# Kernel tuning notes

Hardware: AMD Instinct MI355X
Metric: run time of the kernel (lower is better)

## Reference

```python
import jax, jax.numpy as jnp
import numpy as np

B, T, K, D, H, HL, S, KN = 4096, 50, 32, 64, 256, 128, 100000, 1000


def setup_inputs() -> dict:
    key = jax.random.key(0)
    ks = jax.random.split(key, 24)
    inp = {
        "uididx": jax.random.randint(ks[0], (B,), 0, S, dtype=jnp.int32),
        "kcodeidx": jax.random.randint(ks[1], (B, K), 0, KN, dtype=jnp.int32),
        "kcode_len": jax.random.randint(ks[2], (B,), 1, K + 1, dtype=jnp.int32),
        "qidemb": jax.random.normal(ks[3], (B, T, D), dtype=jnp.float32),
        "qid_len": jax.random.randint(ks[4], (B,), 1, T + 1, dtype=jnp.int32),
        # embedding tables
        "stuE": jax.random.normal(ks[5], (S, D), dtype=jnp.float32) * 0.1,
        "knE": jax.random.normal(ks[6], (KN, D), dtype=jnp.float32) * 0.1,
        # Theta DNN params
        "T_W1": jax.random.normal(ks[7], (D, H), dtype=jnp.float32) * (1.0 / np.sqrt(D)),
        "T_b1": jnp.zeros((H,), jnp.float32),
        "T_W2": jax.random.normal(ks[8], (H, 1), dtype=jnp.float32) * (1.0 / np.sqrt(H)),
        "T_b2": jnp.zeros((1,), jnp.float32),
        # A DNN params
        "A_W1": jax.random.normal(ks[9], (D, H), dtype=jnp.float32) * (1.0 / np.sqrt(D)),
        "A_b1": jnp.zeros((H,), jnp.float32),
        "A_W2": jax.random.normal(ks[10], (H, 1), dtype=jnp.float32) * (1.0 / np.sqrt(H)),
        "A_b2": jnp.zeros((1,), jnp.float32),
        # LSTM params (gate order i,f,g,o) + output head
        "L_Wi": jax.random.normal(ks[11], (D, 4 * HL), dtype=jnp.float32) * (1.0 / np.sqrt(D)),
        "L_Wh": jax.random.normal(ks[12], (HL, 4 * HL), dtype=jnp.float32) * (1.0 / np.sqrt(HL)),
        "L_b": jnp.zeros((4 * HL,), jnp.float32),
        "L_Wo": jax.random.normal(ks[13], (HL, 1), dtype=jnp.float32) * (1.0 / np.sqrt(HL)),
        "L_bo": jnp.zeros((1,), jnp.float32),
    }
    return inp


def _dnn(x, W1, b1, W2, b2):
    return jnp.tanh(x @ W1 + b1) @ W2 + b2


def _lstm_last(x, lengths, Wi, Wh, b):
    # x: [B,T,D]; returns last valid hidden state [B,HL]
    xg = jnp.einsum('btd,dh->bth', x, Wi) + b  # precomputed input projections
    h0 = jnp.zeros((x.shape[0], Wh.shape[0]), x.dtype)

    def step(carry, inp):
        h, c = carry
        g_x, t = inp
        g = g_x + h @ Wh
        i, f, gg, o = jnp.split(g, 4, axis=-1)
        c2 = jax.nn.sigmoid(f) * c + jax.nn.sigmoid(i) * jnp.tanh(gg)
        h2 = jax.nn.sigmoid(o) * jnp.tanh(c2)
        upd = (t < lengths)[:, None]
        return (jnp.where(upd, h2, h), jnp.where(upd, c2, c)), None

    (h, _), _ = jax.lax.scan(step, (h0, h0), (xg.transpose(1, 0, 2), jnp.arange(x.shape[1])))
    return h


def reference(uididx, kcodeidx, kcode_len, qidemb, qid_len, stuE, knE,
              T_W1, T_b1, T_W2, T_b2, A_W1, A_b1, A_W2, A_b2,
              L_Wi, L_Wh, L_b, L_Wo, L_bo):
    stu = stuE[uididx]            # [B,D]
    kemb = knE[kcodeidx]          # [B,K,D]
    kmask = jnp.arange(kcodeidx.shape[1])[None, :] < kcode_len[:, None]  # [B,K]
    kmf = kmask.astype(kemb.dtype)

    # per-student mastery: sigmoid(kemb @ stu / 5), then masked reductions
    mastery = jax.nn.sigmoid(jnp.einsum('bkd,bd->bk', kemb, stu) / 5.0)
    mastvec = jnp.einsum('bk,bkd->bd', mastery * kmf, kemb)  # sum(mastery * kemb)
    avec = jnp.einsum('bk,bkd->bd', kmf, kemb)               # sum(kemb)

    # scaled dot-product attention: q=qidemb, k=v=kemb, scale=0.15
    scores = jnp.einsum('btd,bkd->btk', qidemb, kemb) * 0.15
    scores = jnp.where(kmask[:, None, :], scores, -1e9)
    attw = jax.nn.softmax(scores, axis=-1)
    bvec = jnp.einsum('btk,bkd->btd', attw, kemb)            # [B,T,D]

    t = _dnn(mastvec, T_W1, T_b1, T_W2, T_b2)                             # theta [B,1]
    a = 8.0 * (jax.nn.sigmoid(jnp.abs(_dnn(avec, A_W1, A_b1, A_W2, A_b2))) - 0.5)
    hT = _lstm_last(bvec, qid_len, L_Wi, L_Wh, L_b)
    b = 8.0 * (jax.nn.sigmoid(hT @ L_Wo + L_bo) - 0.5)                    # [B,1]

    return jax.nn.sigmoid(a * (t - b))  # IRT response probability [B,1]
```

## Files before the change

### kernel.cpp

```cpp
#include <hip/hip_runtime.h>
#include <math.h>

#define B_  4096
#define T_  50
#define K_  32
#define D_  64
#define H_  256
#define HL_ 128
#define G4_ 512

typedef __attribute__((ext_vector_type(8))) short bf16x8;
typedef __attribute__((ext_vector_type(4))) float f32x4;

__device__ __forceinline__ float fast_exp(float x){ return __expf(x); }
__device__ __forceinline__ float fast_rcp(float x){ return __builtin_amdgcn_rcpf(x); }
__device__ __forceinline__ float sigmoidf_(float x){ return fast_rcp(1.f + fast_exp(-x)); }
__device__ __forceinline__ float tanhf_(float x){ return 1.f - 2.f*fast_rcp(1.f + fast_exp(2.f*x)); }

__device__ __forceinline__ short f2bf(float f){
  union { float f; unsigned u; } v; v.f = f;
  unsigned r = v.u + 0x7FFFu + ((v.u >> 16) & 1u);
  return (short)(r >> 16);
}
__device__ __forceinline__ float bf2f(short s){
  union { unsigned u; float f; } v; v.u = ((unsigned)(unsigned short)s) << 16;
  return v.f;
}

__device__ __forceinline__ float wave_reduce_sum(float v){
  #pragma unroll
  for (int off = 32; off; off >>= 1) v += __shfl_xor(v, off);
  return v;
}

#define KROW 72
#define PROW 40

__global__ __launch_bounds__(256) void head_kernel(
    const int* __restrict__ uididx, const int* __restrict__ kcodeidx,
    const int* __restrict__ kcode_len, const float* __restrict__ qidemb,
    const int* __restrict__ qid_len, const float* __restrict__ stuE,
    const float* __restrict__ knE,
    const float* __restrict__ T_W1, const float* __restrict__ T_b1,
    const float* __restrict__ T_W2, const float* __restrict__ T_b2,
    const float* __restrict__ A_W1, const float* __restrict__ A_b1,
    const float* __restrict__ A_W2, const float* __restrict__ A_b2,
    short* __restrict__ bvec, float* __restrict__ t_val, float* __restrict__ a_val)
{
  __shared__ __align__(16) short s_kemb[K_*KROW];
  __shared__ __align__(16) short s_kembT[D_*PROW];
  __shared__ __align__(16) short s_p[64*PROW];
  __shared__ float s_stu[D_];
  __shared__ float s_mast[K_];
  __shared__ float s_kmf[K_];
  __shared__ float s_mvec[D_];
  __shared__ float s_avec[D_];
  __shared__ float s_redT[4];
  __shared__ float s_redA[4];

  const int b    = blockIdx.x;
  const int tid  = threadIdx.x;
  const int lane = tid & 63;
  const int w    = tid >> 6;
  const int l15  = lane & 15;
  const int quad = lane >> 4;
  const int klen = kcode_len[b];
  const int qlen = qid_len[b];

  if (tid < D_) s_stu[tid] = stuE[uididx[b]*D_ + tid];
  #pragma unroll
  for (int i = tid; i < 512; i += 256){
    int k = i >> 4, f4 = i & 15;
    const float4 v = *(const float4*)&knE[(size_t)kcodeidx[b*K_ + k]*D_ + f4*4];
    short4 b4; b4.x = f2bf(v.x); b4.y = f2bf(v.y); b4.z = f2bf(v.z); b4.w = f2bf(v.w);
    *(short4*)&s_kemb[k*KROW + f4*4] = b4;
    int d = f4*4;
    s_kembT[(d+0)*PROW + k] = b4.x;
    s_kembT[(d+1)*PROW + k] = b4.y;
    s_kembT[(d+2)*PROW + k] = b4.z;
    s_kembT[(d+3)*PROW + k] = b4.w;
  }
  __syncthreads();

  {
    int k = tid >> 3, l8 = tid & 7;
    float s = 0.f;
    #pragma unroll
    for (int j = 0; j < 8; ++j){
      int d = l8 + 8*((j + k) & 7);
      s += s_stu[d] * bf2f(s_kemb[k*KROW + d]);
    }
    s += __shfl_xor(s, 1); s += __shfl_xor(s, 2); s += __shfl_xor(s, 4);
    if (l8 == 0){
      float valid = (k < klen) ? 1.f : 0.f;
      s_mast[k] = valid * sigmoidf_(s * 0.2f);
      s_kmf[k]  = valid;
    }
  }
  __syncthreads();

  if (tid < D_){
    float mv = 0.f, av = 0.f;
    #pragma unroll 4
    for (int k = 0; k < K_; ++k){
      float e = bf2f(s_kemb[k*KROW + tid]);
      mv += s_mast[k] * e;
      av += s_kmf[k]  * e;
    }
    s_mvec[tid] = mv; s_avec[tid] = av;
  }
  __syncthreads();

  {
    const int qrow = w*16 + l15;
    bf16x8 aq[2];
    #pragma unroll
    for (int kt = 0; kt < 2; ++kt){
      if (qrow < qlen){
        const float4 v0 = *(const float4*)&qidemb[((size_t)b*T_ + qrow)*D_ + kt*32 + quad*8];
        const float4 v1 = *(const float4*)&qidemb[((size_t)b*T_ + qrow)*D_ + kt*32 + quad*8 + 4];
        aq[kt][0]=f2bf(v0.x); aq[kt][1]=f2bf(v0.y); aq[kt][2]=f2bf(v0.z); aq[kt][3]=f2bf(v0.w);
        aq[kt][4]=f2bf(v1.x); aq[kt][5]=f2bf(v1.y); aq[kt][6]=f2bf(v1.z); aq[kt][7]=f2bf(v1.w);
      } else {
        aq[kt][0]=0; aq[kt][1]=0; aq[kt][2]=0; aq[kt][3]=0;
        aq[kt][4]=0; aq[kt][5]=0; aq[kt][6]=0; aq[kt][7]=0;
      }
    }
    f32x4 zero = {0.f, 0.f, 0.f, 0.f};
    f32x4 accs[2] = {zero, zero};
    #pragma unroll
    for (int kt = 0; kt < 2; ++kt){
      #pragma unroll
      for (int nt = 0; nt < 2; ++nt){
        bf16x8 bk = *(const bf16x8*)&s_kemb[(nt*16 + l15)*KROW + kt*32 + quad*8];
        accs[nt] = __builtin_amdgcn_mfma_f32_16x16x32_bf16(aq[kt], bk, accs[nt], 0, 0, 0);
      }
    }
    #pragma unroll
    for (int r = 0; r < 4; ++r){
      float v0 = (l15      < klen) ? accs[0][r]*0.15f : -1e9f;
      float v1 = (l15 + 16 < klen) ? accs[1][r]*0.15f : -1e9f;
      float mx = fmaxf(v0, v1);
      #pragma unroll
      for (int off = 1; off < 16; off <<= 1) mx = fmaxf(mx, __shfl_xor(mx, off));
      float e0 = fast_exp(v0 - mx), e1 = fast_exp(v1 - mx);
      float sm = e0 + e1;
      #pragma unroll
      for (int off = 1; off < 16; off <<= 1) sm += __shfl_xor(sm, off);
      float inv = fast_rcp(sm);
      int row = w*16 + quad*4 + r;
      s_p[row*PROW + l15]      = f2bf(e0 * inv);
      s_p[row*PROW + 16 + l15] = f2bf(e1 * inv);
    }
    bf16x8 ap = *(const bf16x8*)&s_p[(w*16 + l15)*PROW + quad*8];
    #pragma unroll
    for (int nt = 0; nt < 4; ++nt){
      bf16x8 bv = *(const bf16x8*)&s_kembT[(nt*16 + l15)*PROW + quad*8];
      f32x4 acco = __builtin_amdgcn_mfma_f32_16x16x32_bf16(ap, bv, zero, 0, 0, 0);
      #pragma unroll
      for (int r = 0; r < 4; ++r){
        int t = w*16 + quad*4 + r;
        if (t < qlen) bvec[((size_t)b*T_ + t)*D_ + nt*16 + l15] = f2bf(acco[r]);
      }
    }
  }

  {
    float accT = T_b1[tid];
    float accA = A_b1[tid];
    #pragma unroll 4
    for (int d = 0; d < D_; ++d){
      float mv = s_mvec[d], av = s_avec[d];
      accT += mv * T_W1[d*H_ + tid];
      accA += av * A_W1[d*H_ + tid];
    }
    float termT = tanhf_(accT) * T_W2[tid];
    float termA = tanhf_(accA) * A_W2[tid];
    termT = wave_reduce_sum(termT);
    termA = wave_reduce_sum(termA);
    if (lane == 0){ s_redT[w] = termT; s_redA[w] = termA; }
    __syncthreads();
    if (tid == 0){
      t_val[b] = s_redT[0] + s_redT[1] + s_redT[2] + s_redT[3] + T_b2[0];
      float v = s_redA[0] + s_redA[1] + s_redA[2] + s_redA[3] + A_b2[0];
      a_val[b] = 8.f * (sigmoidf_(fabsf(v)) - 0.5f);
    }
  }
}

#define HROW 280

__global__ __launch_bounds__(512) void lstm_kernel(
    const short* __restrict__ bvec, const int* __restrict__ qid_len,
    const float* __restrict__ L_Wi, const float* __restrict__ L_Wh,
    const float* __restrict__ L_b,  const float* __restrict__ L_Wo,
    const float* __restrict__ L_bo, const float* __restrict__ t_val,
    const float* __restrict__ a_val, float* __restrict__ out)
{
  __shared__ __align__(16) short s_A[16*HROW];
  __shared__ int s_len[16];

  const int tid  = threadIdx.x;
  const int s0   = blockIdx.x * 16;
  const int w    = tid >> 6;
  const int lane = tid & 63;
  const int l15  = lane & 15;
  const int quad = lane >> 4;

  bf16x8 wf[4][6];
  f32x4  biasv4[4];
  #pragma unroll
  for (int g = 0; g < 4; ++g){
    const int col = g*128 + w*16 + l15;
    #pragma unroll
    for (int r = 0; r < 4; ++r) biasv4[g][r] = L_b[g*128 + w*16 + quad*4 + r];
    #pragma unroll
    for (int kt = 0; kt < 6; ++kt){
      #pragma unroll
      for (int j = 0; j < 8; ++j){
        int k = kt*32 + quad*8 + j;
        float v = (k < D_) ? L_Wi[k*G4_ + col] : L_Wh[(k-D_)*G4_ + col];
        wf[g][kt][j] = f2bf(v);
      }
    }
  }

  for (int p = tid; p < 16*HROW; p += 512) s_A[p] = 0;
  if (tid < 16) s_len[tid] = qid_len[s0 + tid];
  __syncthreads();

  int maxlen = 0;
  #pragma unroll
  for (int i = 0; i < 16; ++i) maxlen = max(maxlen, s_len[i]);
  const int mylen = s_len[l15];
  float c_reg[4] = {0.f,0.f,0.f,0.f};
  float h_reg[4] = {0.f,0.f,0.f,0.f};

  const short* gx = bvec + (size_t)(s0 + l15)*T_*D_ + quad*8;
  bf16x8 xA0 = *(const bf16x8*)(gx);
  bf16x8 xA1 = *(const bf16x8*)(gx + 32);
  bf16x8 xB0 = xA0, xB1 = xA1;
  if (1 < maxlen){ xB0 = *(const bf16x8*)(gx + D_); xB1 = *(const bf16x8*)(gx + D_ + 32); }
  __syncthreads();

#define MF(Aop, Bop, Cop) __builtin_amdgcn_mfma_f32_16x16x32_bf16((Aop), (Bop), (Cop), 0, 0, 0)

#define LSTM_STEP(TI, XB, XC0, XC1) do {                                       \
    const int hb_ = (XB) ^ 1;                                                  \
    const bf16x8 ah0 = *(const bf16x8*)&s_A[l15*HROW + hb_*128 +  0 + quad*8]; \
    const bf16x8 ah1 = *(const bf16x8*)&s_A[l15*HROW + hb_*128 + 32 + quad*8]; \
    const bf16x8 ah2 = *(const bf16x8*)&s_A[l15*HROW + hb_*128 + 64 + quad*8]; \
    const bf16x8 ah3 = *(const bf16x8*)&s_A[l15*HROW + hb_*128 + 96 + quad*8]; \
    f32x4 a0_ = biasv4[0], a1_ = biasv4[1], a2_ = biasv4[2], a3_ = biasv4[3];  \
    a0_ = MF(wf[0][0], XC0, a0_); a0_ = MF(wf[0][1], XC1, a0_);                \
    a1_ = MF(wf[1][0], XC0, a1_); a1_ = MF(wf[1][1], XC1, a1_);                \
    a2_ = MF(wf[2][0], XC0, a2_); a2_ = MF(wf[2][1], XC1, a2_);                \
    a3_ = MF(wf[3][0], XC0, a3_); a3_ = MF(wf[3][1], XC1, a3_);                \
    if ((TI) + 2 < maxlen){                                                    \
      XC0 = *(const bf16x8*)(gx + ((TI)+2)*D_);                                \
      XC1 = *(const bf16x8*)(gx + ((TI)+2)*D_ + 32);                           \
    }                                                                          \
    a0_ = MF(wf[0][2], ah0, a0_); a0_ = MF(wf[0][3], ah1, a0_);                \
    a0_ = MF(wf[0][4], ah2, a0_); a0_ = MF(wf[0][5], ah3, a0_);                \
    a1_ = MF(wf[1][2], ah0, a1_); a1_ = MF(wf[1][3], ah1, a1_);                \
    a1_ = MF(wf[1][4], ah2, a1_); a1_ = MF(wf[1][5], ah3, a1_);                \
    float si_[4], sf_[4], tg_[4], so_[4];                                      \
    _Pragma("unroll") for (int r = 0; r < 4; ++r) si_[r] = sigmoidf_(a0_[r]);  \
    a2_ = MF(wf[2][2], ah0, a2_); a2_ = MF(wf[2][3], ah1, a2_);                \
    a2_ = MF(wf[2][4], ah2, a2_); a2_ = MF(wf[2][5], ah3, a2_);                \
    _Pragma("unroll") for (int r = 0; r < 4; ++r) sf_[r] = sigmoidf_(a1_[r]);  \
    a3_ = MF(wf[3][2], ah0, a3_); a3_ = MF(wf[3][3], ah1, a3_);                \
    a3_ = MF(wf[3][4], ah2, a3_); a3_ = MF(wf[3][5], ah3, a3_);                \
    _Pragma("unroll") for (int r = 0; r < 4; ++r) tg_[r] = tanhf_(a2_[r]);     \
    _Pragma("unroll") for (int r = 0; r < 4; ++r) so_[r] = sigmoidf_(a3_[r]);  \
    const bool upd_ = (TI) < mylen;                                            \
    _Pragma("unroll")                                                          \
    for (int r = 0; r < 4; ++r){                                               \
      float c2 = sf_[r]*c_reg[r] + si_[r]*tg_[r];                              \
      float h2 = so_[r]*tanhf_(c2);                                            \
      c_reg[r] = upd_ ? c2 : c_reg[r];                                         \
      h_reg[r] = upd_ ? h2 : h_reg[r];                                         \
    }                                                                          \
    uint2 hp_;                                                                 \
    hp_.x = (unsigned)(unsigned short)f2bf(h_reg[0])                           \
          | ((unsigned)(unsigned short)f2bf(h_reg[1]) << 16);                  \
    hp_.y = (unsigned)(unsigned short)f2bf(h_reg[2])                           \
          | ((unsigned)(unsigned short)f2bf(h_reg[3]) << 16);                  \
    *(uint2*)&s_A[l15*HROW + (XB)*128 + w*16 + quad*4] = hp_;                  \
    __syncthreads();                                                           \
  } while(0)

  int t = 0;
  for (; t + 1 < maxlen; t += 2){
    LSTM_STEP(t,   0, xA0, xA1);
    LSTM_STEP(t+1, 1, xB0, xB1);
  }
  if (t < maxlen) LSTM_STEP(t, 0, xA0, xA1);
#undef LSTM_STEP
#undef MF

  const int xbLast = (maxlen - 1) & 1;
  for (int s2 = w; s2 < 16; s2 += 8){
    float h0 = bf2f(s_A[s2*HROW + xbLast*128 + lane]);
    float h1 = bf2f(s_A[s2*HROW + xbLast*128 + 64 + lane]);
    float part = h0*L_Wo[lane] + h1*L_Wo[64+lane];
    part = wave_reduce_sum(part);
    if (lane == 0){
      float bb = 8.f * (sigmoidf_(part + L_bo[0]) - 0.5f);
      out[s0+s2] = sigmoidf_(a_val[s0+s2] * (t_val[s0+s2] - bb));
    }
  }
}

extern "C" void kernel_launch(void* const* d_in, const int* in_sizes, int n_in,
                              void* d_out, int out_size, void* d_ws, size_t ws_size,
                              hipStream_t stream)
{
  (void)in_sizes; (void)n_in; (void)out_size; (void)ws_size;
  const int*   uididx    = (const int*)  d_in[0];
  const int*   kcodeidx  = (const int*)  d_in[1];
  const int*   kcode_len = (const int*)  d_in[2];
  const float* qidemb    = (const float*)d_in[3];
  const int*   qid_len   = (const int*)  d_in[4];
  const float* stuE      = (const float*)d_in[5];
  const float* knE       = (const float*)d_in[6];
  const float* T_W1      = (const float*)d_in[7];
  const float* T_b1      = (const float*)d_in[8];
  const float* T_W2      = (const float*)d_in[9];
  const float* T_b2      = (const float*)d_in[10];
  const float* A_W1      = (const float*)d_in[11];
  const float* A_b1      = (const float*)d_in[12];
  const float* A_W2      = (const float*)d_in[13];
  const float* A_b2      = (const float*)d_in[14];
  const float* L_Wi      = (const float*)d_in[15];
  const float* L_Wh      = (const float*)d_in[16];
  const float* L_b       = (const float*)d_in[17];
  const float* L_Wo      = (const float*)d_in[18];
  const float* L_bo      = (const float*)d_in[19];
  float* out = (float*)d_out;

  short* bvec  = (short*)d_ws;
  float* t_val = (float*)(bvec + (size_t)B_*T_*D_);
  float* a_val = t_val + B_;

  hipLaunchKernelGGL(head_kernel, dim3(B_), dim3(256), 0, stream,
    uididx, kcodeidx, kcode_len, qidemb, qid_len, stuE, knE,
    T_W1, T_b1, T_W2, T_b2, A_W1, A_b1, A_W2, A_b2,
    bvec, t_val, a_val);

  hipLaunchKernelGGL(lstm_kernel, dim3(B_/16), dim3(512), 0, stream,
    bvec, qid_len, L_Wi, L_Wh, L_b, L_Wo, L_bo, t_val, a_val, out);
}
```

Baseline: 219.1 us.

## Software-pipeline LSTM input projection into previous step and use raw barrier

Moves the input-projection MFMAs for step t+1 to the end of step t, after the hidden state is written and before the barrier. The next step then only has to do the recurrent h·Wh MFMAs after the barrier, which shortens the serial critical path. It also replaces __syncthreads with an explicit lgkmcnt wait plus s_barrier between sched_barriers, so the barrier no longer waits on outstanding global loads. The cost is more register pressure and fragile hand scheduling. Dropping the initial __syncthreads relies on the later barriers to order the s_A zeroing.

New measurement: 218.7 us. Within noise of the previous version (-0.2%).

```diff
diff --git a/kernel.cpp b/kernel.cpp
--- a/kernel.cpp
+++ b/kernel.cpp
@@ -241,25 +241,21 @@
   bf16x8 xA1 = *(const bf16x8*)(gx + 32);
   bf16x8 xB0 = xA0, xB1 = xA1;
   if (1 < maxlen){ xB0 = *(const bf16x8*)(gx + D_); xB1 = *(const bf16x8*)(gx + D_ + 32); }
-  __syncthreads();
 
 #define MF(Aop, Bop, Cop) __builtin_amdgcn_mfma_f32_16x16x32_bf16((Aop), (Bop), (Cop), 0, 0, 0)
 
-#define LSTM_STEP(TI, XB, XC0, XC1) do {                                       \
+  f32x4 a0_ = MF(wf[0][0], xA0, biasv4[0]); a0_ = MF(wf[0][1], xA1, a0_);
+  f32x4 a1_ = MF(wf[1][0], xA0, biasv4[1]); a1_ = MF(wf[1][1], xA1, a1_);
+  f32x4 a2_ = MF(wf[2][0], xA0, biasv4[2]); a2_ = MF(wf[2][1], xA1, a2_);
+  f32x4 a3_ = MF(wf[3][0], xA0, biasv4[3]); a3_ = MF(wf[3][1], xA1, a3_);
+  if (2 < maxlen){ xA0 = *(const bf16x8*)(gx + 2*D_); xA1 = *(const bf16x8*)(gx + 2*D_ + 32); }
+
+#define LSTM_STEP(TI, XB, XN0, XN1) do {                                       \
     const int hb_ = (XB) ^ 1;                                                  \
     const bf16x8 ah0 = *(const bf16x8*)&s_A[l15*HROW + hb_*128 +  0 + quad*8]; \
     const bf16x8 ah1 = *(const bf16x8*)&s_A[l15*HROW + hb_*128 + 32 + quad*8]; \
     const bf16x8 ah2 = *(const bf16x8*)&s_A[l15*HROW + hb_*128 + 64 + quad*8]; \
     const bf16x8 ah3 = *(const bf16x8*)&s_A[l15*HROW + hb_*128 + 96 + quad*8]; \
-    f32x4 a0_ = biasv4[0], a1_ = biasv4[1], a2_ = biasv4[2], a3_ = biasv4[3];  \
-    a0_ = MF(wf[0][0], XC0, a0_); a0_ = MF(wf[0][1], XC1, a0_);                \
-    a1_ = MF(wf[1][0], XC0, a1_); a1_ = MF(wf[1][1], XC1, a1_);                \
-    a2_ = MF(wf[2][0], XC0, a2_); a2_ = MF(wf[2][1], XC1, a2_);                \
-    a3_ = MF(wf[3][0], XC0, a3_); a3_ = MF(wf[3][1], XC1, a3_);                \
-    if ((TI) + 2 < maxlen){                                                    \
-      XC0 = *(const bf16x8*)(gx + ((TI)+2)*D_);                                \
-      XC1 = *(const bf16x8*)(gx + ((TI)+2)*D_ + 32);                           \
-    }                                                                          \
     a0_ = MF(wf[0][2], ah0, a0_); a0_ = MF(wf[0][3], ah1, a0_);                \
     a0_ = MF(wf[0][4], ah2, a0_); a0_ = MF(wf[0][5], ah3, a0_);                \
     a1_ = MF(wf[1][2], ah0, a1_); a1_ = MF(wf[1][3], ah1, a1_);                \
@@ -287,15 +283,27 @@
     hp_.y = (unsigned)(unsigned short)f2bf(h_reg[2])                           \
           | ((unsigned)(unsigned short)f2bf(h_reg[3]) << 16);                  \
     *(uint2*)&s_A[l15*HROW + (XB)*128 + w*16 + quad*4] = hp_;                  \
-    __syncthreads();                                                           \
+         \
+    a0_ = MF(wf[0][0], XN0, biasv4[0]); a0_ = MF(wf[0][1], XN1, a0_);          \
+    a1_ = MF(wf[1][0], XN0, biasv4[1]); a1_ = MF(wf[1][1], XN1, a1_);          \
+    a2_ = MF(wf[2][0], XN0, biasv4[2]); a2_ = MF(wf[2][1], XN1, a2_);          \
+    a3_ = MF(wf[3][0], XN0, biasv4[3]); a3_ = MF(wf[3][1], XN1, a3_);          \
+    if ((TI) + 3 < maxlen){                                                    \
+      XN0 = *(const bf16x8*)(gx + ((TI)+3)*D_);                                \
+      XN1 = *(const bf16x8*)(gx + ((TI)+3)*D_ + 32);                           \
+    }                                                                          \
+    __builtin_amdgcn_sched_barrier(0);                                         \
+    asm volatile("s_waitcnt lgkmcnt(0)" ::: "memory");                         \
+    __builtin_amdgcn_s_barrier();                                              \
+    __builtin_amdgcn_sched_barrier(0);                                         \
   } while(0)
 
   int t = 0;
   for (; t + 1 < maxlen; t += 2){
-    LSTM_STEP(t,   0, xA0, xA1);
-    LSTM_STEP(t+1, 1, xB0, xB1);
-  }
-  if (t < maxlen) LSTM_STEP(t, 0, xA0, xA1);
+    LSTM_STEP(t,   0, xB0, xB1);
+    LSTM_STEP(t+1, 1, xA0, xA1);
+  }
+  if (t < maxlen) LSTM_STEP(t, 0, xB0, xB1);
 #undef LSTM_STEP
 #undef MF
 
```

## Process 8 sequences per LSTM block with duplicated MFMA rows to double grid

Applied to the files above, without the earlier changes.

The LSTM kernel now handles 8 sequences per block instead of 16, so the grid grows to 512 blocks. Each 16-row MFMA tile carries every sequence twice, and each lane does the gate nonlinearities for only 2 of its 4 accumulator rows. A launch-bounds occupancy hint of 4 is added. The aim is to fill more compute units and shorten each lane's serial activation work per step, at the cost of wasting half of the MFMA throughput and loading the weights in twice as many blocks.

Measured after the change: 593.1 us. 171% more time.

```diff
diff --git a/kernel.cpp b/kernel.cpp
--- a/kernel.cpp
+++ b/kernel.cpp
@@ -190,22 +190,24 @@
 
 #define HROW 280
 
-__global__ __launch_bounds__(512) void lstm_kernel(
+__global__ __launch_bounds__(512, 4) void lstm_kernel(
     const short* __restrict__ bvec, const int* __restrict__ qid_len,
     const float* __restrict__ L_Wi, const float* __restrict__ L_Wh,
     const float* __restrict__ L_b,  const float* __restrict__ L_Wo,
     const float* __restrict__ L_bo, const float* __restrict__ t_val,
     const float* __restrict__ a_val, float* __restrict__ out)
 {
-  __shared__ __align__(16) short s_A[16*HROW];
-  __shared__ int s_len[16];
+  __shared__ __align__(16) short s_A[8*HROW];
+  __shared__ int s_len[8];
 
   const int tid  = threadIdx.x;
-  const int s0   = blockIdx.x * 16;
+  const int s0   = blockIdx.x * 8;
   const int w    = tid >> 6;
   const int lane = tid & 63;
   const int l15  = lane & 15;
   const int quad = lane >> 4;
+  const int st8  = l15 & 7;
+  const int rb   = (l15 >> 3) * 2;
 
   bf16x8 wf[4][6];
   f32x4  biasv4[4];
@@ -225,18 +227,18 @@
     }
   }
 
-  for (int p = tid; p < 16*HROW; p += 512) s_A[p] = 0;
-  if (tid < 16) s_len[tid] = qid_len[s0 + tid];
+  for (int p = tid; p < 8*HROW; p += 512) s_A[p] = 0;
+  if (tid < 8) s_len[tid] = qid_len[s0 + tid];
   __syncthreads();
 
   int maxlen = 0;
   #pragma unroll
-  for (int i = 0; i < 16; ++i) maxlen = max(maxlen, s_len[i]);
-  const int mylen = s_len[l15];
-  float c_reg[4] = {0.f,0.f,0.f,0.f};
-  float h_reg[4] = {0.f,0.f,0.f,0.f};
-
-  const short* gx = bvec + (size_t)(s0 + l15)*T_*D_ + quad*8;
+  for (int i = 0; i < 8; ++i) maxlen = max(maxlen, s_len[i]);
+  const int mylen = s_len[st8];
+  float c_reg[2] = {0.f, 0.f};
+  float h_reg[2] = {0.f, 0.f};
+
+  const short* gx = bvec + (size_t)(s0 + st8)*T_*D_ + quad*8;
   bf16x8 xA0 = *(const bf16x8*)(gx);
   bf16x8 xA1 = *(const bf16x8*)(gx + 32);
   bf16x8 xB0 = xA0, xB1 = xA1;
@@ -247,10 +249,10 @@
 
 #define LSTM_STEP(TI, XB, XC0, XC1) do {                                       \
     const int hb_ = (XB) ^ 1;                                                  \
-    const bf16x8 ah0 = *(const bf16x8*)&s_A[l15*HROW + hb_*128 +  0 + quad*8]; \
-    const bf16x8 ah1 = *(const bf16x8*)&s_A[l15*HROW + hb_*128 + 32 + quad*8]; \
-    const bf16x8 ah2 = *(const bf16x8*)&s_A[l15*HROW + hb_*128 + 64 + quad*8]; \
-    const bf16x8 ah3 = *(const bf16x8*)&s_A[l15*HROW + hb_*128 + 96 + quad*8]; \
+    const bf16x8 ah0 = *(const bf16x8*)&s_A[st8*HROW + hb_*128 +  0 + quad*8]; \
+    const bf16x8 ah1 = *(const bf16x8*)&s_A[st8*HROW + hb_*128 + 32 + quad*8]; \
+    const bf16x8 ah2 = *(const bf16x8*)&s_A[st8*HROW + hb_*128 + 64 + quad*8]; \
+    const bf16x8 ah3 = *(const bf16x8*)&s_A[st8*HROW + hb_*128 + 96 + quad*8]; \
     f32x4 a0_ = biasv4[0], a1_ = biasv4[1], a2_ = biasv4[2], a3_ = biasv4[3];  \
     a0_ = MF(wf[0][0], XC0, a0_); a0_ = MF(wf[0][1], XC1, a0_);                \
     a1_ = MF(wf[1][0], XC0, a1_); a1_ = MF(wf[1][1], XC1, a1_);                \
@@ -264,29 +266,23 @@
     a0_ = MF(wf[0][4], ah2, a0_); a0_ = MF(wf[0][5], ah3, a0_);                \
     a1_ = MF(wf[1][2], ah0, a1_); a1_ = MF(wf[1][3], ah1, a1_);                \
     a1_ = MF(wf[1][4], ah2, a1_); a1_ = MF(wf[1][5], ah3, a1_);                \
-    float si_[4], sf_[4], tg_[4], so_[4];                                      \
-    _Pragma("unroll") for (int r = 0; r < 4; ++r) si_[r] = sigmoidf_(a0_[r]);  \
     a2_ = MF(wf[2][2], ah0, a2_); a2_ = MF(wf[2][3], ah1, a2_);                \
     a2_ = MF(wf[2][4], ah2, a2_); a2_ = MF(wf[2][5], ah3, a2_);                \
-    _Pragma("unroll") for (int r = 0; r < 4; ++r) sf_[r] = sigmoidf_(a1_[r]);  \
     a3_ = MF(wf[3][2], ah0, a3_); a3_ = MF(wf[3][3], ah1, a3_);                \
     a3_ = MF(wf[3][4], ah2, a3_); a3_ = MF(wf[3][5], ah3, a3_);                \
-    _Pragma("unroll") for (int r = 0; r < 4; ++r) tg_[r] = tanhf_(a2_[r]);     \
-    _Pragma("unroll") for (int r = 0; r < 4; ++r) so_[r] = sigmoidf_(a3_[r]);  \
     const bool upd_ = (TI) < mylen;                                            \
     _Pragma("unroll")                                                          \
-    for (int r = 0; r < 4; ++r){                                               \
-      float c2 = sf_[r]*c_reg[r] + si_[r]*tg_[r];                              \
-      float h2 = so_[r]*tanhf_(c2);                                            \
-      c_reg[r] = upd_ ? c2 : c_reg[r];                                         \
-      h_reg[r] = upd_ ? h2 : h_reg[r];                                         \
+    for (int k = 0; k < 2; ++k){                                               \
+      const int r = rb + k;                                                    \
+      float gi = a0_[r], gf = a1_[r], gg = a2_[r], go = a3_[r];                \
+      float c2 = sigmoidf_(gf)*c_reg[k] + sigmoidf_(gi)*tanhf_(gg);            \
+      float h2 = sigmoidf_(go)*tanhf_(c2);                                     \
+      c_reg[k] = upd_ ? c2 : c_reg[k];                                         \
+      h_reg[k] = upd_ ? h2 : h_reg[k];                                         \
     }                                                                          \
-    uint2 hp_;                                                                 \
-    hp_.x = (unsigned)(unsigned short)f2bf(h_reg[0])                           \
-          | ((unsigned)(unsigned short)f2bf(h_reg[1]) << 16);                  \
-    hp_.y = (unsigned)(unsigned short)f2bf(h_reg[2])                           \
-          | ((unsigned)(unsigned short)f2bf(h_reg[3]) << 16);                  \
-    *(uint2*)&s_A[l15*HROW + (XB)*128 + w*16 + quad*4] = hp_;                  \
+    unsigned hp_ = (unsigned)(unsigned short)f2bf(h_reg[0])                    \
+                 | ((unsigned)(unsigned short)f2bf(h_reg[1]) << 16);           \
+    *(unsigned*)&s_A[st8*HROW + (XB)*128 + w*16 + quad*4 + rb] = hp_;          \
     __syncthreads();                                                           \
   } while(0)
 
@@ -300,7 +296,8 @@
 #undef MF
 
   const int xbLast = (maxlen - 1) & 1;
-  for (int s2 = w; s2 < 16; s2 += 8){
+  if (w < 8){
+    const int s2 = w;
     float h0 = bf2f(s_A[s2*HROW + xbLast*128 + lane]);
     float h1 = bf2f(s_A[s2*HROW + xbLast*128 + 64 + lane]);
     float part = h0*L_Wo[lane] + h1*L_Wo[64+lane];
@@ -348,6 +345,6 @@
     T_W1, T_b1, T_W2, T_b2, A_W1, A_b1, A_W2, A_b2,
     bvec, t_val, a_val);
 
-  hipLaunchKernelGGL(lstm_kernel, dim3(B_/16), dim3(512), 0, stream,
+  hipLaunchKernelGGL(lstm_kernel, dim3(B_/8), dim3(512), 0, stream,
     bvec, qid_len, L_Wi, L_Wh, L_b, L_Wo, L_bo, t_val, a_val, out);
 }
```

## Move theta/A DNN heads from head kernel into LSTM kernel with batched weight reuse

Applied to the files above, without the earlier changes.

Moves the two small MLP heads (theta and A) out of the per-sample head kernel and into the LSTM kernel. There, each block handles 16 samples, and each thread computes 8 hidden columns with float4 weight loads. The head kernel now writes mastvec and avecs to global memory instead of doing its own 64x256 matvecs per sample. This is meant to cut the repeated W1 weight traffic and shorten the head kernel, which does one block per sample. The cost is an extra global round-trip for the two vectors and extra serial work at the start of the LSTM kernel.

Measured after the change: 225.6 us. 2.9% more time.

```diff
diff --git a/kernel.cpp b/kernel.cpp
--- a/kernel.cpp
+++ b/kernel.cpp
@@ -41,11 +41,7 @@
     const int* __restrict__ kcode_len, const float* __restrict__ qidemb,
     const int* __restrict__ qid_len, const float* __restrict__ stuE,
     const float* __restrict__ knE,
-    const float* __restrict__ T_W1, const float* __restrict__ T_b1,
-    const float* __restrict__ T_W2, const float* __restrict__ T_b2,
-    const float* __restrict__ A_W1, const float* __restrict__ A_b1,
-    const float* __restrict__ A_W2, const float* __restrict__ A_b2,
-    short* __restrict__ bvec, float* __restrict__ t_val, float* __restrict__ a_val)
+    short* __restrict__ bvec, float* __restrict__ mvecG, float* __restrict__ avecG)
 {
   __shared__ __align__(16) short s_kemb[K_*KROW];
   __shared__ __align__(16) short s_kembT[D_*PROW];
@@ -53,10 +49,6 @@
   __shared__ float s_stu[D_];
   __shared__ float s_mast[K_];
   __shared__ float s_kmf[K_];
-  __shared__ float s_mvec[D_];
-  __shared__ float s_avec[D_];
-  __shared__ float s_redT[4];
-  __shared__ float s_redA[4];
 
   const int b    = blockIdx.x;
   const int tid  = threadIdx.x;
@@ -107,7 +99,8 @@
       mv += s_mast[k] * e;
       av += s_kmf[k]  * e;
     }
-    s_mvec[tid] = mv; s_avec[tid] = av;
+    mvecG[(size_t)b*D_ + tid] = mv;
+    avecG[(size_t)b*D_ + tid] = av;
   }
   __syncthreads();
 
@@ -164,28 +157,6 @@
       }
     }
   }
-
-  {
-    float accT = T_b1[tid];
-    float accA = A_b1[tid];
-    #pragma unroll 4
-    for (int d = 0; d < D_; ++d){
-      float mv = s_mvec[d], av = s_avec[d];
-      accT += mv * T_W1[d*H_ + tid];
-      accA += av * A_W1[d*H_ + tid];
-    }
-    float termT = tanhf_(accT) * T_W2[tid];
-    float termA = tanhf_(accA) * A_W2[tid];
-    termT = wave_reduce_sum(termT);
-    termA = wave_reduce_sum(termA);
-    if (lane == 0){ s_redT[w] = termT; s_redA[w] = termA; }
-    __syncthreads();
-    if (tid == 0){
-      t_val[b] = s_redT[0] + s_redT[1] + s_redT[2] + s_redT[3] + T_b2[0];
-      float v = s_redA[0] + s_redA[1] + s_redA[2] + s_redA[3] + A_b2[0];
-      a_val[b] = 8.f * (sigmoidf_(fabsf(v)) - 0.5f);
-    }
-  }
 }
 
 #define HROW 280
@@ -194,11 +165,18 @@
     const short* __restrict__ bvec, const int* __restrict__ qid_len,
     const float* __restrict__ L_Wi, const float* __restrict__ L_Wh,
     const float* __restrict__ L_b,  const float* __restrict__ L_Wo,
-    const float* __restrict__ L_bo, const float* __restrict__ t_val,
-    const float* __restrict__ a_val, float* __restrict__ out)
+    const float* __restrict__ L_bo,
+    const float* __restrict__ T_W1, const float* __restrict__ T_b1,
+    const float* __restrict__ T_W2, const float* __restrict__ T_b2,
+    const float* __restrict__ A_W1, const float* __restrict__ A_b1,
+    const float* __restrict__ A_W2, const float* __restrict__ A_b2,
+    const float* __restrict__ mvecG, const float* __restrict__ avecG,
+    float* __restrict__ out)
 {
   __shared__ __align__(16) short s_A[16*HROW];
   __shared__ int s_len[16];
+  __shared__ float s_tv[16];
+  __shared__ float s_av[16];
 
   const int tid  = threadIdx.x;
   const int s0   = blockIdx.x * 16;
@@ -206,6 +184,42 @@
   const int lane = tid & 63;
   const int l15  = lane & 15;
   const int quad = lane >> 4;
+
+  {
+    const int sI = tid >> 5;
+    const int c0 = (tid & 31) * 8;
+    const float* mv = mvecG + (size_t)(s0 + sI)*D_;
+    const float* av = avecG + (size_t)(s0 + sI)*D_;
+    float accT[8], accA[8];
+    #pragma unroll
+    for (int j = 0; j < 8; ++j){ accT[j] = T_b1[c0+j]; accA[j] = A_b1[c0+j]; }
+    for (int d = 0; d < D_; ++d){
+      const float m = mv[d], a = av[d];
+      const float4 wT0 = *(const float4*)&T_W1[d*H_ + c0];
+      const float4 wT1 = *(const float4*)&T_W1[d*H_ + c0 + 4];
+      const float4 wA0 = *(const float4*)&A_W1[d*H_ + c0];
+      const float4 wA1 = *(const float4*)&A_W1[d*H_ + c0 + 4];
+      accT[0] += m*wT0.x; accT[1] += m*wT0.y; accT[2] += m*wT0.z; accT[3] += m*wT0.w;
+      accT[4] += m*wT1.x; accT[5] += m*wT1.y; accT[6] += m*wT1.z; accT[7] += m*wT1.w;
+      accA[0] += a*wA0.x; accA[1] += a*wA0.y; accA[2] += a*wA0.z; accA[3] += a*wA0.w;
+      accA[4] += a*wA1.x; accA[5] += a*wA1.y; accA[6] += a*wA1.z; accA[7] += a*wA1.w;
+    }
+    float tT = 0.f, tA = 0.f;
+    #pragma unroll
+    for (int j = 0; j < 8; ++j){
+      tT += tanhf_(accT[j]) * T_W2[c0+j];
+      tA += tanhf_(accA[j]) * A_W2[c0+j];
+    }
+    #pragma unroll
+    for (int off = 1; off < 32; off <<= 1){
+      tT += __shfl_xor(tT, off);
+      tA += __shfl_xor(tA, off);
+    }
+    if ((lane & 31) == 0){
+      s_tv[sI] = tT + T_b2[0];
+      s_av[sI] = 8.f * (sigmoidf_(fabsf(tA + A_b2[0])) - 0.5f);
+    }
+  }
 
   bf16x8 wf[4][6];
   f32x4  biasv4[4];
@@ -307,7 +321,7 @@
     part = wave_reduce_sum(part);
     if (lane == 0){
       float bb = 8.f * (sigmoidf_(part + L_bo[0]) - 0.5f);
-      out[s0+s2] = sigmoidf_(a_val[s0+s2] * (t_val[s0+s2] - bb));
+      out[s0+s2] = sigmoidf_(s_av[s2] * (s_tv[s2] - bb));
     }
   }
 }
@@ -340,14 +354,15 @@
   float* out = (float*)d_out;
 
   short* bvec  = (short*)d_ws;
-  float* t_val = (float*)(bvec + (size_t)B_*T_*D_);
-  float* a_val = t_val + B_;
+  float* mvecG = (float*)(bvec + (size_t)B_*T_*D_);
+  float* avecG = mvecG + (size_t)B_*D_;
 
   hipLaunchKernelGGL(head_kernel, dim3(B_), dim3(256), 0, stream,
     uididx, kcodeidx, kcode_len, qidemb, qid_len, stuE, knE,
+    bvec, mvecG, avecG);
+
+  hipLaunchKernelGGL(lstm_kernel, dim3(B_/16), dim3(512), 0, stream,
+    bvec, qid_len, L_Wi, L_Wh, L_b, L_Wo, L_bo,
     T_W1, T_b1, T_W2, T_b2, A_W1, A_b1, A_W2, A_b2,
-    bvec, t_val, a_val);
-
-  hipLaunchKernelGGL(lstm_kernel, dim3(B_/16), dim3(512), 0, stream,
-    bvec, qid_len, L_Wi, L_Wh, L_b, L_Wo, L_bo, t_val, a_val, out);
-}
+    mvecG, avecG, out);
+}
```
